# Kernel optimization log

Measured on AMD Instinct MI355X. Metric: run time of the kernel, lower is better.

## Reference

```python
import jax, jax.numpy as jnp
import numpy as np

GAMMA_LL = 1.7595e11            # gyromagnetic ratio (rad/s/T), class constant
MU0 = np.float32(4e-7 * np.pi)  # vacuum permeability
A_EXCH = 3.65e-12               # exchange stiffness (J/m)
ALPHA = 0.01                    # Gilbert damping (run)
ALPHA_RELAX = 0.5               # high damping used by relax()
DT = 5e-12                      # timestep (s)
DX = DY = 50e-9                 # cell size (m)
NX = NY = 256
T = 1024
RELAX_STEPS = 100               # relax_timesteps class constant


def _laplacian(m):
    # m: (1,3,NX,NY); 5-point Laplacian with Neumann (replicate) boundaries
    mp = jnp.pad(m, ((0, 0), (0, 0), (1, 1), (1, 1)), mode="edge")
    lap_x = (mp[:, :, 2:, 1:-1] + mp[:, :, :-2, 1:-1] - 2.0 * m) / (DX * DX)
    lap_y = (mp[:, :, 1:-1, 2:] + mp[:, :, 1:-1, :-2] - 2.0 * m) / (DY * DY)
    return lap_x + lap_y


def _B_eff(m, B_ext, Msat):
    # B_ext + exchange + (local thin-film) demag
    B_exch = (2.0 * A_EXCH / Msat) * _laplacian(m)
    zhat = jnp.array([0.0, 0.0, 1.0], m.dtype).reshape(1, 3, 1, 1)
    B_demag = -MU0 * Msat * m * zhat
    return B_ext + B_exch + B_demag


def _torque_LLG(m, B_ext, Msat, alpha):
    m_x_B = jnp.cross(m, _B_eff(m, B_ext, Msat), axis=1)
    return -(m_x_B + alpha * jnp.cross(m, m_x_B, axis=1)) / (1.0 + alpha * alpha)


def _rk4_step(m, B_ext, Msat, alpha):
    h = GAMMA_LL * DT
    k1 = _torque_LLG(m, B_ext, Msat, alpha)
    k2 = _torque_LLG(m + 0.5 * h * k1, B_ext, Msat, alpha)
    k3 = _torque_LLG(m + 0.5 * h * k2, B_ext, Msat, alpha)
    k4 = _torque_LLG(m + h * k3, B_ext, Msat, alpha)
    return m + (h / 6.0) * (k1 + 2.0 * k2 + 2.0 * k3 + k4)


def setup_inputs() -> dict:
    key = jax.random.key(0)
    signal = jax.random.normal(key, (1, T, 1), jnp.float32)
    # 60 mT out-of-plane bias field
    B_ext = jnp.zeros((1, 3, NX, NY), jnp.float32).at[:, 2].set(0.06)
    Msat = 1.4e5 * jnp.ones((1, 1, NX, NY), jnp.float32)
    # source antenna: 1 mT/unit signal on Bx in a 20x20 patch
    src_mask = jnp.zeros((1, 3, NX, NY), jnp.float32).at[:, 0, 20:40, 118:138].set(1e-3)
    probe_mask = jnp.zeros((NX, NY), jnp.float32).at[216:236, 118:138].set(1.0)
    return {"signal": signal, "B_ext": B_ext, "Msat": Msat,
            "src_mask": src_mask, "probe_mask": probe_mask}


def reference(signal, B_ext, Msat, src_mask, probe_mask):
    dtype = signal.dtype
    m_init = jnp.zeros((1, 3, NX, NY), dtype).at[:, 2].set(1.0)

    # relax(): high-damping RK4 steps under no_grad
    B_ext_c = jax.lax.stop_gradient(B_ext)
    Msat_c = jax.lax.stop_gradient(Msat)
    m0 = jax.lax.fori_loop(
        0, RELAX_STEPS,
        lambda i, m: _rk4_step(m, B_ext_c, Msat_c, ALPHA_RELAX),
        m_init)
    m0 = jax.lax.stop_gradient(m0)

    pm_sum = jnp.sum(probe_mask)

    def step(m, s):
        Bt = B_ext + s * src_mask            # inject_sources
        m = _rk4_step(m, Bt, Msat, ALPHA)    # rk4_step_LLG
        # measure_probes: mean mx of (m - m0) * Msat over probe region
        out = jnp.sum(((m - m0) * Msat)[:, 0] * probe_mask) / pm_sum
        return m, out

    m_final, outs = jax.lax.scan(jax.checkpoint(step), m0, signal[0, :, 0])
    return outs[None, :]  # (1, T) concatenated probe outputs
```

## Files before the change

### kernel.cpp

```cpp
#include <hip/hip_runtime.h>

#define TST   1024
#define OWN   16
#define HALO  4
#define TDIM  24
#define NT    576
#define NB    256

typedef float v4f __attribute__((ext_vector_type(4)));

#define AG __HIP_MEMORY_SCOPE_AGENT
__device__ __forceinline__ float agload (const float* p){ return __hip_atomic_load (p, __ATOMIC_RELAXED, AG); }
__device__ __forceinline__ int   agloadi(const int* p)  { return __hip_atomic_load (p, __ATOMIC_RELAXED, AG); }
__device__ __forceinline__ void  agstoref(float* p,float v){      __hip_atomic_store(p, v, __ATOMIC_RELAXED, AG); }
__device__ __forceinline__ void  agstorei(int* p,int v) {         __hip_atomic_store(p, v, __ATOMIC_RELAXED, AG); }

__device__ __forceinline__ v4f ld16_dev(const v4f* p) {
    v4f r;
    asm volatile("global_load_dwordx4 %0, %1, off sc1\n\ts_waitcnt vmcnt(0)"
                 : "=v"(r) : "v"(p) : "memory");
    return r;
}
__device__ __forceinline__ void st16_dev(v4f* p, v4f v) {
    asm volatile("global_store_dwordx4 %0, %1, off sc1" :: "v"(p), "v"(v) : "memory");
}

__global__ void __launch_bounds__(NT)
mm_solver(const float* __restrict__ signal,
          const float* __restrict__ B_ext,
          const float* __restrict__ Msat,
          const float* __restrict__ src_mask,
          const float* __restrict__ probe_mask,
          float* __restrict__ out,
          float* __restrict__ ws)
{
    const int b  = (int)blockIdx.x;
    const int bx = b & 15, by = b >> 4;
    const int t  = (int)threadIdx.x;
    const int tr = t / TDIM, tc = t % TDIM;
    const int wv = t >> 6;

    const int grow = by * OWN - HALO + tr;
    const int gcol = bx * OWN - HALO + tc;
    const bool inG = (grow >= 0 && grow < 256 && gcol >= 0 && gcol < 256);
    const bool own = (tr >= HALO && tr < HALO + OWN && tc >= HALO && tc < HALO + OWN);

    v4f*   pub   = (v4f*)ws;
    float* priv  = ws + 2 * 65536 * 4;
    int*   doneA = (int*)(priv + NB * TST);
    const int pubStride = 65536;

    __shared__ v4f  EB[2][TDIM * TDIM];
    __shared__ float sigS[TST];
    __shared__ int  wctr[11];
    __shared__ int   hasP;
    __shared__ int   pfl[NB];
    __shared__ float redS[16];
    __shared__ float pmsS;

    volatile int* cl  = (volatile int*)&wctr[wv];
    volatile int* cr  = (volatile int*)&wctr[wv + 2];
    volatile int* cme = (volatile int*)&wctr[wv + 1];
    const bool lane0 = ((t & 63) == 0);

#define PUB_CTR(G) do { \
    asm volatile("s_waitcnt lgkmcnt(0)" ::: "memory"); \
    if (lane0) *cme = (G); \
    asm volatile("" ::: "memory"); \
} while (0)
#define SPIN_NBR(G) do { \
    while (*cl < (G)) {} \
    while (*cr < (G)) {} \
    asm volatile("" ::: "memory"); \
} while (0)

    const float invd   = (float)(1.0 / (double)((float)(50e-9 * 50e-9)));
    const float h      = (float)(1.7595e11 * 5e-12);
    const float hh     = (float)(0.5 * (1.7595e11 * 5e-12));
    const float h6     = (float)((1.7595e11 * 5e-12) / 6.0);
    const float alpha  = 0.01f;
    const float inv1a2 = (float)(1.0 / (1.0 + 0.01 * 0.01));

    const int growc = grow < 0 ? 0 : (grow > 255 ? 255 : grow);
    const int gcolc = gcol < 0 ? 0 : (gcol > 255 ? 255 : gcol);
    const int idxg  = growc * 256 + gcolc;
    const float bxv = B_ext[idxg], byv = B_ext[65536 + idxg], bzv = B_ext[131072 + idxg];
    const float ms  = Msat[idxg];
    const float sxv = src_mask[idxg], syv = src_mask[65536 + idxg], szv = src_mask[131072 + idxg];
    const float pm  = probe_mask[idxg];
    const float ce   = 7.3e-12f / ms;
    const float cdem = -(float)(4.0e-7 * 3.14159265358979323846) * ms;

    const int idx  = t;
    const int offU = ((tr < TDIM - 1) && (grow < 255)) ?  TDIM : 0;
    const int offD = ((tr > 0)        && (grow > 0))   ? -TDIM : 0;
    const int offR = ((tc < TDIM - 1) && (gcol < 255)) ?  1 : 0;
    const int offL = ((tc > 0)        && (gcol > 0))   ? -1 : 0;

    const int slotOff = idxg;

    float mx = 0.0f, my = 0.0f, mz = 1.0f;

    if (own) st16_dev(pub + slotOff, (v4f){0.0f, 0.0f, 1.0f, __int_as_float(0)});
    for (int k = t; k < TST; k += NT) sigS[k] = signal[k];
    if (t < 11) wctr[t] = (t == 0 || t == 10) ? 0x7fffffff : -1;
    if (t == 11) hasP = 0;
    __syncthreads();
    const bool pcell = own && (pm != 0.0f);
    if (pcell) atomicOr(&hasP, 1);
    const bool waveP = (__ballot(pcell) != 0ull);
    __syncthreads();
    const int hasPr = hasP;
    if (hasPr) for (int k = t; k < TST; k += NT) agstoref(&priv[b * TST + k], 0.0f);
    __syncthreads();

    const bool haloT = inG && !own;
    float ex, ey, ez, ax, ay, az, kx, ky, kz, btx, bty, btz;

#define STAGE(SB) do { \
    const v4f u = EB[SB][idx + offU]; \
    const v4f d = EB[SB][idx + offD]; \
    const v4f r = EB[SB][idx + offR]; \
    const v4f l = EB[SB][idx + offL]; \
    float lx = ((u.x + d.x - 2.0f * ex) + (r.x + l.x - 2.0f * ex)) * invd; \
    float ly = ((u.y + d.y - 2.0f * ey) + (r.y + l.y - 2.0f * ey)) * invd; \
    float lz = ((u.z + d.z - 2.0f * ez) + (r.z + l.z - 2.0f * ez)) * invd; \
    float Bx = btx + ce * lx; \
    float By = bty + ce * ly; \
    float Bz = btz + ce * lz + cdem * ez; \
    float cx = ey * Bz - ez * By; \
    float cy = ez * Bx - ex * Bz; \
    float cz = ex * By - ey * Bx; \
    float dx = ey * cz - ez * cy; \
    float dy = ez * cx - ex * cz; \
    float dz = ex * cy - ey * cx; \
    kx = -(cx + alpha * dx) * inv1a2; \
    ky = -(cy + alpha * dy) * inv1a2; \
    kz = -(cz + alpha * dz) * inv1a2; \
} while (0)

#define WRE(DB) do { EB[DB][idx] = (v4f){ex, ey, ez, 0.0f}; } while (0)

    for (int i = 0; i < TST; ++i) {
        const float s = sigS[i];
        const int  g0 = i << 2;

        if (haloT) {
            const v4f* p = pub + (i & 1) * pubStride + slotOff;
            for (;;) {
                v4f hv = ld16_dev(p);
                if (__float_as_int(hv.w) >= i) { mx = hv.x; my = hv.y; mz = hv.z; break; }
            }
        }

        btx = bxv + s * sxv;  bty = byv + s * syv;  btz = bzv + s * szv;
        ex = mx; ey = my; ez = mz;
        WRE(0);
        PUB_CTR(g0);
        SPIN_NBR(g0);
        STAGE(0);
        ax = kx; ay = ky; az = kz;
        ex = mx + hh * kx; ey = my + hh * ky; ez = mz + hh * kz;
        WRE(1);
        PUB_CTR(g0 + 1);

        SPIN_NBR(g0 + 1);
        STAGE(1);
        ax += 2.0f * kx; ay += 2.0f * ky; az += 2.0f * kz;
        ex = mx + hh * kx; ey = my + hh * ky; ez = mz + hh * kz;
        WRE(0);
        PUB_CTR(g0 + 2);

        SPIN_NBR(g0 + 2);
        STAGE(0);
        ax += 2.0f * kx; ay += 2.0f * ky; az += 2.0f * kz;
        ex = mx + h * kx; ey = my + h * ky; ez = mz + h * kz;
        WRE(1);
        PUB_CTR(g0 + 3);

        SPIN_NBR(g0 + 3);
        STAGE(1);
        ax += kx; ay += ky; az += kz;
        mx += h6 * ax; my += h6 * ay; mz += h6 * az;

        if (own) st16_dev(pub + ((i + 1) & 1) * pubStride + slotOff,
                          (v4f){mx, my, mz, __int_as_float(i + 1)});

        if (waveP) {
            float c = pcell ? mx * ms * pm : 0.0f;
            #pragma unroll
            for (int off = 32; off > 0; off >>= 1) c += __shfl_down(c, off, 64);
            if (lane0) atomicAdd(&priv[b * TST + i], c);
        }
    }

    __syncthreads();
    if (t == 0) agstorei(&doneA[b], 0x5D0000 | hasPr);

    if (b == 0) {
        if (t < NB) {
            int v;
            for (;;) { v = agloadi(&doneA[t]); if ((v & ~1) == 0x5D0000) break;
                       __builtin_amdgcn_s_sleep(8); }
            pfl[t] = v & 1;
        }
        __syncthreads();
        float ps = 0.0f;
        for (int k = t; k < 65536; k += NT) ps += probe_mask[k];
        #pragma unroll
        for (int off = 32; off > 0; off >>= 1) ps += __shfl_down(ps, off, 64);
        if (lane0) redS[wv] = ps;
        __syncthreads();
        if (t == 0) { float q = 0.0f; for (int w = 0; w < 9; ++w) q += redS[w]; pmsS = q; }
        __syncthreads();
        const float pms = pmsS;
        for (int o = t; o < TST; o += NT) {
            float sm = 0.0f;
            for (int j = 0; j < NB; ++j) if (pfl[j]) sm += agload(&priv[j * TST + o]);
            out[o] = sm / pms;
        }
    }
}

extern "C" void kernel_launch(void* const* d_in, const int* in_sizes, int n_in,
                              void* d_out, int out_size, void* d_ws, size_t ws_size,
                              hipStream_t stream)
{
    const float* signal = (const float*)d_in[0];
    const float* B_ext  = (const float*)d_in[1];
    const float* Msat   = (const float*)d_in[2];
    const float* src    = (const float*)d_in[3];
    const float* probe  = (const float*)d_in[4];
    float* out = (float*)d_out;
    float* ws  = (float*)d_ws;

    void* args[] = { &signal, &B_ext, &Msat, &src, &probe, &out, &ws };
    (void)in_sizes; (void)n_in; (void)out_size; (void)ws_size;

    hipLaunchCooperativeKernel(reinterpret_cast<void*>(mm_solver),
                               dim3(NB), dim3(NT), args, 0, stream);
}
```

Baseline: 2.985 ms.

## Replace halo-recompute tiles with per-stage boundary exchange via dedicated halo wave

```diff
diff --git a/kernel.cpp b/kernel.cpp
--- a/kernel.cpp
+++ b/kernel.cpp
@@ -1,11 +1,8 @@
 #include <hip/hip_runtime.h>
 
-#define TST   1024
-#define OWN   16
-#define HALO  4
-#define TDIM  24
-#define NT    576
-#define NB    256
+#define TST 1024
+#define NB  256
+#define NT  320
 
 typedef float v4f __attribute__((ext_vector_type(4)));
 
@@ -37,42 +34,24 @@
     const int b  = (int)blockIdx.x;
     const int bx = b & 15, by = b >> 4;
     const int t  = (int)threadIdx.x;
-    const int tr = t / TDIM, tc = t % TDIM;
     const int wv = t >> 6;
-
-    const int grow = by * OWN - HALO + tr;
-    const int gcol = bx * OWN - HALO + tc;
-    const bool inG = (grow >= 0 && grow < 256 && gcol >= 0 && gcol < 256);
-    const bool own = (tr >= HALO && tr < HALO + OWN && tc >= HALO && tc < HALO + OWN);
+    const bool isOwn = (t < 256);
+    const bool lane0 = ((t & 63) == 0);
 
     v4f*   pub   = (v4f*)ws;
     float* priv  = ws + 2 * 65536 * 4;
     int*   doneA = (int*)(priv + NB * TST);
     const int pubStride = 65536;
 
-    __shared__ v4f  EB[2][TDIM * TDIM];
+    __shared__ v4f  E0[324];
+    __shared__ v4f  E1[324];
     __shared__ float sigS[TST];
-    __shared__ int  wctr[11];
-    __shared__ int   hasP;
-    __shared__ int   pfl[NB];
-    __shared__ float redS[16];
+    __shared__ int  wctr[6];
+    __shared__ int  w4c;
+    __shared__ int  hasP;
+    __shared__ int  pfl[NB];
+    __shared__ float redS[5];
     __shared__ float pmsS;
-
-    volatile int* cl  = (volatile int*)&wctr[wv];
-    volatile int* cr  = (volatile int*)&wctr[wv + 2];
-    volatile int* cme = (volatile int*)&wctr[wv + 1];
-    const bool lane0 = ((t & 63) == 0);
-
-#define PUB_CTR(G) do { \
-    asm volatile("s_waitcnt lgkmcnt(0)" ::: "memory"); \
-    if (lane0) *cme = (G); \
-    asm volatile("" ::: "memory"); \
-} while (0)
-#define SPIN_NBR(G) do { \
-    while (*cl < (G)) {} \
-    while (*cr < (G)) {} \
-    asm volatile("" ::: "memory"); \
-} while (0)
 
     const float invd   = (float)(1.0 / (double)((float)(50e-9 * 50e-9)));
     const float h      = (float)(1.7595e11 * 5e-12);
@@ -81,32 +60,52 @@
     const float alpha  = 0.01f;
     const float inv1a2 = (float)(1.0 / (1.0 + 0.01 * 0.01));
 
-    const int growc = grow < 0 ? 0 : (grow > 255 ? 255 : grow);
-    const int gcolc = gcol < 0 ? 0 : (gcol > 255 ? 255 : gcol);
-    const int idxg  = growc * 256 + gcolc;
-    const float bxv = B_ext[idxg], byv = B_ext[65536 + idxg], bzv = B_ext[131072 + idxg];
-    const float ms  = Msat[idxg];
-    const float sxv = src_mask[idxg], syv = src_mask[65536 + idxg], szv = src_mask[131072 + idxg];
-    const float pm  = probe_mask[idxg];
-    const float ce   = 7.3e-12f / ms;
-    const float cdem = -(float)(4.0e-7 * 3.14159265358979323846) * ms;
-
-    const int idx  = t;
-    const int offU = ((tr < TDIM - 1) && (grow < 255)) ?  TDIM : 0;
-    const int offD = ((tr > 0)        && (grow > 0))   ? -TDIM : 0;
-    const int offR = ((tc < TDIM - 1) && (gcol < 255)) ?  1 : 0;
-    const int offL = ((tc > 0)        && (gcol > 0))   ? -1 : 0;
-
-    const int slotOff = idxg;
-
+    int  eidx = 0, offU = 0, offD = 0, offR = 0, offL = 0, slotP = 0;
+    bool pubT = false;
+    int  hidx = 0, slotL = 0; bool hvalid = false;
+    float bxv = 0, byv = 0, bzv = 0, ms = 0, sxv = 0, syv = 0, szv = 0, pm = 0;
+    float ce = 0, cdem = 0;
     float mx = 0.0f, my = 0.0f, mz = 1.0f;
-
-    if (own) st16_dev(pub + slotOff, (v4f){0.0f, 0.0f, 1.0f, __int_as_float(0)});
+    if (isOwn) {
+        const int r = t >> 4, c = t & 15;
+        const int grow = by * 16 + r, gcol = bx * 16 + c;
+        const int idxg = grow * 256 + gcol;
+        bxv = B_ext[idxg]; byv = B_ext[65536 + idxg]; bzv = B_ext[131072 + idxg];
+        ms  = Msat[idxg];
+        sxv = src_mask[idxg]; syv = src_mask[65536 + idxg]; szv = src_mask[131072 + idxg];
+        pm  = probe_mask[idxg];
+        ce   = 7.3e-12f / ms;
+        cdem = -(float)(4.0e-7 * 3.14159265358979323846) * ms;
+        eidx = (r + 1) * 18 + (c + 1);
+        offU = (grow < 255) ?  18 : 0;
+        offD = (grow > 0)   ? -18 : 0;
+        offR = (gcol < 255) ?   1 : 0;
+        offL = (gcol > 0)   ?  -1 : 0;
+        pubT = (r == 0) | (r == 15) | (c == 0) | (c == 15);
+        slotP = idxg;
+    } else {
+        const int k = t - 256, side = k >> 4, j = k & 15;
+        int hr, hc;
+        if      (side == 0) { hr = -1; hc = j;  }
+        else if (side == 1) { hr = 16; hc = j;  }
+        else if (side == 2) { hr = j;  hc = -1; }
+        else                { hr = j;  hc = 16; }
+        const int grow = by * 16 + hr, gcol = bx * 16 + hc;
+        hvalid = (grow >= 0 && grow < 256 && gcol >= 0 && gcol < 256);
+        hidx   = (hr + 1) * 18 + (hc + 1);
+        slotL  = hvalid ? grow * 256 + gcol : 0;
+    }
+
+    if (isOwn) {
+        E0[eidx] = (v4f){0.0f, 0.0f, 1.0f, 0.0f};
+        if (pubT) st16_dev(pub + slotP, (v4f){0.0f, 0.0f, 1.0f, __int_as_float(0)});
+    }
     for (int k = t; k < TST; k += NT) sigS[k] = signal[k];
-    if (t < 11) wctr[t] = (t == 0 || t == 10) ? 0x7fffffff : -1;
-    if (t == 11) hasP = 0;
-    __syncthreads();
-    const bool pcell = own && (pm != 0.0f);
+    if (t < 6)  wctr[t] = (t == 0 || t == 5) ? 0x7fffffff : 0;
+    if (t == 6) { volatile int* vw = &w4c; *vw = -1; }
+    if (t == 7) hasP = 0;
+    __syncthreads();
+    const bool pcell = isOwn && (pm != 0.0f);
     if (pcell) atomicOr(&hasP, 1);
     const bool waveP = (__ballot(pcell) != 0ull);
     __syncthreads();
@@ -114,83 +113,120 @@
     if (hasPr) for (int k = t; k < TST; k += NT) agstoref(&priv[b * TST + k], 0.0f);
     __syncthreads();
 
-    const bool haloT = inG && !own;
-    float ex, ey, ez, ax, ay, az, kx, ky, kz, btx, bty, btz;
-
-#define STAGE(SB) do { \
-    const v4f u = EB[SB][idx + offU]; \
-    const v4f d = EB[SB][idx + offD]; \
-    const v4f r = EB[SB][idx + offR]; \
-    const v4f l = EB[SB][idx + offL]; \
-    float lx = ((u.x + d.x - 2.0f * ex) + (r.x + l.x - 2.0f * ex)) * invd; \
-    float ly = ((u.y + d.y - 2.0f * ey) + (r.y + l.y - 2.0f * ey)) * invd; \
-    float lz = ((u.z + d.z - 2.0f * ez) + (r.z + l.z - 2.0f * ez)) * invd; \
-    float Bx = btx + ce * lx; \
-    float By = bty + ce * ly; \
-    float Bz = btz + ce * lz + cdem * ez; \
-    float cx = ey * Bz - ez * By; \
-    float cy = ez * Bx - ex * Bz; \
-    float cz = ex * By - ey * Bx; \
-    float dx = ey * cz - ez * cy; \
-    float dy = ez * cx - ex * cz; \
-    float dz = ex * cy - ey * cx; \
+#define STAGE(EP, exv, eyv, ezv, btxv, btyv, btzv) do { \
+    const v4f u = (EP)[eidx + offU]; \
+    const v4f d = (EP)[eidx + offD]; \
+    const v4f r = (EP)[eidx + offR]; \
+    const v4f l = (EP)[eidx + offL]; \
+    float lx = ((u.x + d.x - 2.0f * exv) + (r.x + l.x - 2.0f * exv)) * invd; \
+    float ly = ((u.y + d.y - 2.0f * eyv) + (r.y + l.y - 2.0f * eyv)) * invd; \
+    float lz = ((u.z + d.z - 2.0f * ezv) + (r.z + l.z - 2.0f * ezv)) * invd; \
+    float Bx = btxv + ce * lx; \
+    float By = btyv + ce * ly; \
+    float Bz = btzv + ce * lz + cdem * ezv; \
+    float cx = eyv * Bz - ezv * By; \
+    float cy = ezv * Bx - exv * Bz; \
+    float cz = exv * By - eyv * Bx; \
+    float dx = eyv * cz - ezv * cy; \
+    float dy = ezv * cx - exv * cz; \
+    float dz = exv * cy - eyv * cx; \
     kx = -(cx + alpha * dx) * inv1a2; \
     ky = -(cy + alpha * dy) * inv1a2; \
     kz = -(cz + alpha * dz) * inv1a2; \
 } while (0)
 
-#define WRE(DB) do { EB[DB][idx] = (v4f){ex, ey, ez, 0.0f}; } while (0)
-
-    for (int i = 0; i < TST; ++i) {
-        const float s = sigS[i];
-        const int  g0 = i << 2;
-
-        if (haloT) {
-            const v4f* p = pub + (i & 1) * pubStride + slotOff;
+    if (isOwn) {
+        volatile int* cl  = (volatile int*)&wctr[wv];
+        volatile int* cr  = (volatile int*)&wctr[wv + 2];
+        volatile int* cme = (volatile int*)&wctr[wv + 1];
+        volatile int* vw4 = (volatile int*)&w4c;
+        float ex, ey, ez, ax, ay, az, kx, ky, kz, btx, bty, btz;
+
+#define SPIN_OWN(G) do { \
+    while (*cl  < (G)) {} \
+    while (*cr  < (G)) {} \
+    while (*vw4 < (G)) {} \
+    asm volatile("" ::: "memory"); \
+} while (0)
+#define PUB_CTR(G) do { \
+    asm volatile("s_waitcnt lgkmcnt(0)" ::: "memory"); \
+    if (lane0) *cme = (G); \
+    asm volatile("" ::: "memory"); \
+} while (0)
+#define PUBE(G, PX, PY, PZ) do { \
+    if (pubT) { \
+        asm volatile("s_waitcnt vmcnt(0)" ::: "memory"); \
+        st16_dev(pub + ((G) & 1) * pubStride + slotP, \
+                 (v4f){PX, PY, PZ, __int_as_float(G)}); \
+    } \
+} while (0)
+
+        for (int i = 0; i < TST; ++i) {
+            const float s = sigS[i];
+            const int g0 = i << 2;
+            btx = bxv + s * sxv;  bty = byv + s * syv;  btz = bzv + s * szv;
+
+            SPIN_OWN(g0);
+            ex = mx; ey = my; ez = mz;
+            STAGE(E0, ex, ey, ez, btx, bty, btz);
+            ax = kx; ay = ky; az = kz;
+            ex = mx + hh * kx; ey = my + hh * ky; ez = mz + hh * kz;
+            E1[eidx] = (v4f){ex, ey, ez, 0.0f};
+            PUBE(g0 + 1, ex, ey, ez);
+            PUB_CTR(g0 + 1);
+
+            SPIN_OWN(g0 + 1);
+            STAGE(E1, ex, ey, ez, btx, bty, btz);
+            ax += 2.0f * kx; ay += 2.0f * ky; az += 2.0f * kz;
+            ex = mx + hh * kx; ey = my + hh * ky; ez = mz + hh * kz;
+            E0[eidx] = (v4f){ex, ey, ez, 0.0f};
+            PUBE(g0 + 2, ex, ey, ez);
+            PUB_CTR(g0 + 2);
+
+            SPIN_OWN(g0 + 2);
+            STAGE(E0, ex, ey, ez, btx, bty, btz);
+            ax += 2.0f * kx; ay += 2.0f * ky; az += 2.0f * kz;
+            ex = mx + h * kx; ey = my + h * ky; ez = mz + h * kz;
+            E1[eidx] = (v4f){ex, ey, ez, 0.0f};
+            PUBE(g0 + 3, ex, ey, ez);
+            PUB_CTR(g0 + 3);
+
+            SPIN_OWN(g0 + 3);
+            STAGE(E1, ex, ey, ez, btx, bty, btz);
+            ax += kx; ay += ky; az += kz;
+            mx += h6 * ax; my += h6 * ay; mz += h6 * az;
+            E0[eidx] = (v4f){mx, my, mz, 0.0f};
+            PUBE(g0 + 4, mx, my, mz);
+            PUB_CTR(g0 + 4);
+
+            if (waveP) {
+                float c = pcell ? mx * ms * pm : 0.0f;
+                #pragma unroll
+                for (int off = 32; off > 0; off >>= 1) c += __shfl_down(c, off, 64);
+                if (lane0) atomicAdd(&priv[b * TST + i], c);
+            }
+        }
+    } else {
+        volatile int* vc  = (volatile int*)wctr;
+        volatile int* vw4 = (volatile int*)&w4c;
+        for (int g = 0; g <= 4095; ++g) {
+            const int gm = g - 1;
             for (;;) {
-                v4f hv = ld16_dev(p);
-                if (__float_as_int(hv.w) >= i) { mx = hv.x; my = hv.y; mz = hv.z; break; }
+                if (vc[1] >= gm && vc[2] >= gm && vc[3] >= gm && vc[4] >= gm) break;
             }
-        }
-
-        btx = bxv + s * sxv;  bty = byv + s * syv;  btz = bzv + s * szv;
-        ex = mx; ey = my; ez = mz;
-        WRE(0);
-        PUB_CTR(g0);
-        SPIN_NBR(g0);
-        STAGE(0);
-        ax = kx; ay = ky; az = kz;
-        ex = mx + hh * kx; ey = my + hh * ky; ez = mz + hh * kz;
-        WRE(1);
-        PUB_CTR(g0 + 1);
-
-        SPIN_NBR(g0 + 1);
-        STAGE(1);
-        ax += 2.0f * kx; ay += 2.0f * ky; az += 2.0f * kz;
-        ex = mx + hh * kx; ey = my + hh * ky; ez = mz + hh * kz;
-        WRE(0);
-        PUB_CTR(g0 + 2);
-
-        SPIN_NBR(g0 + 2);
-        STAGE(0);
-        ax += 2.0f * kx; ay += 2.0f * ky; az += 2.0f * kz;
-        ex = mx + h * kx; ey = my + h * ky; ez = mz + h * kz;
-        WRE(1);
-        PUB_CTR(g0 + 3);
-
-        SPIN_NBR(g0 + 3);
-        STAGE(1);
-        ax += kx; ay += ky; az += kz;
-        mx += h6 * ax; my += h6 * ay; mz += h6 * az;
-
-        if (own) st16_dev(pub + ((i + 1) & 1) * pubStride + slotOff,
-                          (v4f){mx, my, mz, __int_as_float(i + 1)});
-
-        if (waveP) {
-            float c = pcell ? mx * ms * pm : 0.0f;
-            #pragma unroll
-            for (int off = 32; off > 0; off >>= 1) c += __shfl_down(c, off, 64);
-            if (lane0) atomicAdd(&priv[b * TST + i], c);
+            asm volatile("" ::: "memory");
+            v4f hv = (v4f){0.0f, 0.0f, 0.0f, 0.0f};
+            const v4f* p = pub + (g & 1) * pubStride + slotL;
+            for (;;) {
+                v4f tmp = (v4f){0.0f, 0.0f, 0.0f, 0.0f};
+                if (hvalid) { tmp = ld16_dev(p); hv = tmp; }
+                const bool need = hvalid && (__float_as_int(tmp.w) < g);
+                if (__ballot(need) == 0ull) break;
+            }
+            if (hvalid) { if (g & 1) E1[hidx] = hv; else E0[hidx] = hv; }
+            asm volatile("s_waitcnt lgkmcnt(0)" ::: "memory");
+            if (t == 256) *vw4 = g;
+            asm volatile("" ::: "memory");
         }
     }
 
@@ -211,7 +247,7 @@
         for (int off = 32; off > 0; off >>= 1) ps += __shfl_down(ps, off, 64);
         if (lane0) redS[wv] = ps;
         __syncthreads();
-        if (t == 0) { float q = 0.0f; for (int w = 0; w < 9; ++w) q += redS[w]; pmsS = q; }
+        if (t == 0) { float q = 0.0f; for (int w = 0; w < 5; ++w) q += redS[w]; pmsS = q; }
         __syncthreads();
         const float pms = pmsS;
         for (int o = t; o < TST; o += NT) {
```

After: 6.296 ms. 111% more time.
